# Kernel optimization log

Measured on AMD Instinct MI355X. Metric: run time of the kernel, lower is better.

Reference implementation:

```python
import jax, jax.numpy as jnp
import numpy as np
import math

D_MODEL = 1024
D_HEAD = 128
B, T = 4, 4096


def setup_inputs() -> dict:
    key = jax.random.key(0)
    ks = jax.random.split(key, 7)
    x = jax.random.normal(ks[0], (B, T, D_MODEL), dtype=jnp.float32)
    # realistic RoPE tables for positions 0..T-1, d_head//2 frequencies
    half = D_HEAD // 2
    inv_freq = 1.0 / (10000.0 ** (np.arange(0, half, dtype=np.float32) / half))
    pos = np.arange(T, dtype=np.float32)
    ang = pos[:, None] * inv_freq[None, :]  # [T, half]
    cos = jnp.asarray(np.cos(ang), dtype=jnp.float32)
    sin = jnp.asarray(np.sin(ang), dtype=jnp.float32)
    scale = 1.0 / math.sqrt(D_MODEL)
    Wq = jax.random.normal(ks[1], (D_MODEL, D_HEAD), dtype=jnp.float32) * scale
    Wk = jax.random.normal(ks[2], (D_MODEL, D_HEAD), dtype=jnp.float32) * scale
    Wv = jax.random.normal(ks[3], (D_MODEL, D_HEAD), dtype=jnp.float32) * scale
    gamma = jnp.zeros((D_HEAD,), dtype=jnp.float32)
    return {"x": x, "cos": cos, "sin": sin, "Wq": Wq, "Wk": Wk, "Wv": Wv, "gamma": gamma}


def _rotary(t, cos, sin):
    # t: [B, T, d_head]; cos/sin: [T, d_head//2]
    t1 = t[..., ::2]
    t2 = t[..., 1::2]
    r1 = t1 * cos - t2 * sin
    r2 = t1 * sin + t2 * cos
    # interleave back: stack on new last axis then flatten
    return jnp.stack([r1, r2], axis=-1).reshape(t.shape)


def reference(x, cos, sin, Wq, Wk, Wv, gamma):
    d_head = Wq.shape[-1]
    Q = x @ Wq  # [B, T, d_head]
    K = x @ Wk
    V = x @ Wv
    Qr = _rotary(Q, cos, sin)
    Kr = _rotary(K, cos, sin)
    gate = jnp.exp(gamma)  # SPD gate
    Qr = Qr * gate
    Kr = Kr * gate
    scores = jnp.einsum('btd,bsd->bts', Qr, Kr) / math.sqrt(d_head)
    attn = jax.nn.softmax(scores, axis=-1)
    out = jnp.einsum('bts,bsd->btd', attn, V)
    return out
```

## Files before the change

kernel.cpp:

```cpp
#include <hip/hip_runtime.h>

typedef _Float16 h8  __attribute__((ext_vector_type(8)));
typedef float f32x16 __attribute__((ext_vector_type(16)));

#define L2E 1.4426950408889634f

__device__ __forceinline__ void gll16(const void* g, void* l) {
  __builtin_amdgcn_global_load_lds((const __attribute__((address_space(1))) void*)g,
                                   (__attribute__((address_space(3))) void*)l, 16, 0, 0);
}

__global__ void k_cvt_x(const float* __restrict__ x, _Float16* __restrict__ xh) {
  int i = (blockIdx.x * 256 + threadIdx.x) * 8;
  float4 a = *(const float4*)(x + i);
  float4 b = *(const float4*)(x + i + 4);
  h8 o;
  o[0] = (_Float16)a.x; o[1] = (_Float16)a.y; o[2] = (_Float16)a.z; o[3] = (_Float16)a.w;
  o[4] = (_Float16)b.x; o[5] = (_Float16)b.y; o[6] = (_Float16)b.z; o[7] = (_Float16)b.w;
  *(h8*)(xh + i) = o;
}

__global__ void k_cvt_w(const float* __restrict__ Wq, const float* __restrict__ Wk,
                        const float* __restrict__ Wv, _Float16* __restrict__ WT) {
  int id = blockIdx.x * 256 + threadIdx.x;
  int mat = id >> 17;
  int rem = id & 131071;
  int k = rem >> 7;
  int c = rem & 127;
  const float* W = (mat == 0) ? Wq : ((mat == 1) ? Wk : Wv);
  WT[mat * 131072 + c * 1024 + k] = (_Float16)W[rem];
}

__global__ __launch_bounds__(256, 2) void k_proj(
    const _Float16* __restrict__ xh,
    const _Float16* __restrict__ WT,
    const float* __restrict__ cosT, const float* __restrict__ sinT,
    const float* __restrict__ gamma,
    _Float16* __restrict__ Qh, _Float16* __restrict__ Kh, _Float16* __restrict__ VT) {
  __shared__ __align__(16) unsigned char lds[65536];
  const int tid = threadIdx.x;
  const int rt  = blockIdx.x & 127;
  const int mat = blockIdx.x >> 7;
  const int w = tid >> 6, lane = tid & 63;
  const int wr = w >> 1, wc = w & 1;
  const int r32 = lane & 31, h = lane >> 5;
  const int row0 = rt * 128;
  const _Float16* Wbase = WT + mat * 131072;

  auto stage = [&](int j) {
    int k0 = j * 64;
    unsigned char* xb = lds + (j & 1) * 32768;
    unsigned char* wb = xb + 16384;
#pragma unroll
    for (int ii = 0; ii < 4; ++ii) {
      int off = ii * 4096 + tid * 16;
      int r = off >> 7;
      int c = (off >> 4) & 7;
      gll16(xh + (size_t)(row0 + r) * 1024 + k0 + ((c ^ (r & 7)) * 8), xb + off);
    }
#pragma unroll
    for (int ii = 0; ii < 4; ++ii) {
      int off = ii * 4096 + tid * 16;
      int r = off >> 7;
      int c = (off >> 4) & 7;
      gll16(Wbase + (size_t)r * 1024 + k0 + ((c ^ (r & 7)) * 8), wb + off);
    }
  };

  f32x16 acc[2][2];
#pragma unroll
  for (int a_ = 0; a_ < 2; ++a_)
#pragma unroll
    for (int b_ = 0; b_ < 2; ++b_)
#pragma unroll
      for (int r = 0; r < 16; ++r) acc[a_][b_][r] = 0.f;

  stage(0);
  for (int j = 0; j < 16; ++j) {
    if (j < 15) {
      stage(j + 1);
      asm volatile("s_waitcnt vmcnt(8)\n\ts_barrier" ::: "memory");
    } else {
      asm volatile("s_waitcnt vmcnt(0)\n\ts_barrier" ::: "memory");
    }
    const _Float16* xt = (const _Float16*)(lds + (j & 1) * 32768);
    const _Float16* wt = xt + 8192;
#pragma unroll
    for (int kk = 0; kk < 4; ++kk) {
      h8 a0, a1, b0, b1;
      { int r = wr * 64 + r32;      a0 = *(const h8*)(xt + r * 64 + (((kk * 2 + h) ^ (r & 7)) * 8)); }
      { int r = wr * 64 + 32 + r32; a1 = *(const h8*)(xt + r * 64 + (((kk * 2 + h) ^ (r & 7)) * 8)); }
      { int r = wc * 64 + r32;      b0 = *(const h8*)(wt + r * 64 + (((kk * 2 + h) ^ (r & 7)) * 8)); }
      { int r = wc * 64 + 32 + r32; b1 = *(const h8*)(wt + r * 64 + (((kk * 2 + h) ^ (r & 7)) * 8)); }
      acc[0][0] = __builtin_amdgcn_mfma_f32_32x32x16_f16(a0, b0, acc[0][0], 0, 0, 0);
      acc[0][1] = __builtin_amdgcn_mfma_f32_32x32x16_f16(a0, b1, acc[0][1], 0, 0, 0);
      acc[1][0] = __builtin_amdgcn_mfma_f32_32x32x16_f16(a1, b0, acc[1][0], 0, 0, 0);
      acc[1][1] = __builtin_amdgcn_mfma_f32_32x32x16_f16(a1, b1, acc[1][1], 0, 0, 0);
    }
    asm volatile("s_waitcnt lgkmcnt(0)\n\ts_barrier" ::: "memory");
  }

#pragma unroll
  for (int mt = 0; mt < 2; ++mt)
#pragma unroll
    for (int nt = 0; nt < 2; ++nt) {
      int col = wc * 64 + nt * 32 + r32;
      f32x16 c = acc[mt][nt];
      if (mat < 2) {
        float ge = expf(gamma[col]);
        float sc = (mat == 0) ? ge * 0.08838834764831845f : ge;
        int i2 = col >> 1;
#pragma unroll
        for (int rg = 0; rg < 16; ++rg) {
          int row = row0 + wr * 64 + mt * 32 + (rg & 3) + 8 * (rg >> 2) + 4 * h;
          int pos = row & 4095;
          float cv = cosT[pos * 64 + i2], sv = sinT[pos * 64 + i2];
          float val = c[rg];
          float ot = __shfl_xor(val, 1);
          float rr = (lane & 1) ? fmaf(val, cv, ot * sv) : fmaf(val, cv, -ot * sv);
          float v = rr * sc;
          if (mat == 0) {
            Qh[(size_t)row * 128 + col] = (_Float16)v;
          } else {
            size_t ka = (size_t)(row >> 5) * 4096 + (col >> 4) * 512 +
                        ((col >> 3) & 1) * 256 + (row & 31) * 8 + (col & 7);
            Kh[ka] = (_Float16)v;
          }
        }
      } else {
#pragma unroll
        for (int g = 0; g < 4; ++g) {
          union { _Float16 hh[4]; uint2 u; } pk;
#pragma unroll
          for (int j2 = 0; j2 < 4; ++j2) pk.hh[j2] = (_Float16)c[g * 4 + j2];
          int kv = row0 + wr * 64 + mt * 32 + 8 * g + 4 * h;
          size_t va = (size_t)(kv >> 5) * 4096 +
                      ((col >> 5) * 2 + ((kv >> 4) & 1)) * 512 +
                      ((kv >> 3) & 1) * 256 + (col & 31) * 8 + (kv & 7);
          *(uint2*)(VT + va) = pk.u;
        }
      }
    }
}

__global__ __launch_bounds__(512, 2) void k_attn(
    const _Float16* __restrict__ Qh, const _Float16* __restrict__ Kh,
    const _Float16* __restrict__ VT, float* __restrict__ out) {
  extern __shared__ __align__(16) unsigned char lds_raw[];
  const int tid = threadIdx.x;
  const int bid = blockIdx.x;
  const int xcd = bid & 7;
  const int b  = xcd >> 1;
  const int q0 = ((xcd & 1) + 2 * (bid >> 3)) * 64;
  const int w = tid >> 6, lane = tid & 63;
  const int wk = w >> 1, wq = w & 1;
  const int r32 = lane & 31, h = lane >> 5;

  const _Float16* qrow = Qh + (size_t)(b * 4096 + q0 + wq * 32 + r32) * 128;
  h8 qf[8];
#pragma unroll
  for (int kk = 0; kk < 8; ++kk) qf[kk] = *(const h8*)(qrow + kk * 16 + h * 8);

  const _Float16* Kfb = Kh + (size_t)(b * 128 + wk) * 4096 + lane * 8;
  const _Float16* Vfb = VT + (size_t)(b * 128 + wk) * 4096 + lane * 8;

  f32x16 o_acc[4];
#pragma unroll
  for (int dt = 0; dt < 4; ++dt)
#pragma unroll
    for (int r = 0; r < 16; ++r) o_acc[dt][r] = 0.f;
  float mcur = -INFINITY, lsum = 0.f;

  h8 kf[8];
#pragma unroll
  for (int kk = 0; kk < 8; ++kk) kf[kk] = *(const h8*)(Kfb + kk * 512);

  for (int i = 0; i < 32; ++i) {
    __builtin_amdgcn_s_barrier();

    const _Float16* Vcur = Vfb + (size_t)i * 16384;
    h8 vf[8];
#pragma unroll
    for (int u = 0; u < 8; ++u) vf[u] = *(const h8*)(Vcur + u * 512);

    const _Float16* Knext = Kfb + (size_t)(i + 1) * 16384;
    f32x16 st0, st1;
#pragma unroll
    for (int r = 0; r < 16; ++r) { st0[r] = 0.f; st1[r] = 0.f; }
    __builtin_amdgcn_s_setprio(1);
#pragma unroll
    for (int kk = 0; kk < 8; ++kk) {
      h8 a = kf[kk];
      if (i < 31) kf[kk] = *(const h8*)(Knext + kk * 512);
      if (kk & 1) st1 = __builtin_amdgcn_mfma_f32_32x32x16_f16(a, qf[kk], st1, 0, 0, 0);
      else        st0 = __builtin_amdgcn_mfma_f32_32x32x16_f16(a, qf[kk], st0, 0, 0, 0);
    }
    __builtin_amdgcn_s_setprio(0);
    f32x16 st = st0 + st1;

    float pm = fmaxf(fmaxf(fmaxf(st[0], st[1]), fmaxf(st[2], st[3])),
                     fmaxf(fmaxf(st[4], st[5]), fmaxf(st[6], st[7])));
    float pm2 = fmaxf(fmaxf(fmaxf(st[8], st[9]), fmaxf(st[10], st[11])),
                      fmaxf(fmaxf(st[12], st[13]), fmaxf(st[14], st[15])));
    pm = fmaxf(pm, pm2);
    pm = fmaxf(pm, __shfl_xor(pm, 32));
    if (!__all(pm - mcur <= 8.0f)) {
      float mnew = fmaxf(mcur, pm);
      float fsc = exp2f((mcur - mnew) * L2E);
      lsum *= fsc;
#pragma unroll
      for (int dt = 0; dt < 4; ++dt) o_acc[dt] = o_acc[dt] * fsc;
      mcur = mnew;
    }
    float mn2 = mcur * L2E;
    float pv[16]; float ps = 0.f;
#pragma unroll
    for (int r = 0; r < 16; ++r) { pv[r] = exp2f(fmaf(st[r], L2E, -mn2)); ps += pv[r]; }
    ps += __shfl_xor(ps, 32);
    lsum += ps;

    unsigned int wrd[8], owd[8];
#pragma unroll
    for (int t8 = 0; t8 < 8; ++t8) {
      auto hp = __builtin_amdgcn_cvt_pkrtz(pv[2 * t8], pv[2 * t8 + 1]);
      wrd[t8] = __builtin_bit_cast(unsigned int, hp);
    }
#pragma unroll
    for (int t8 = 0; t8 < 8; ++t8) owd[t8] = (unsigned int)__shfl_xor((int)wrd[t8], 32);
    const bool hb = (h != 0);
    __builtin_amdgcn_s_setprio(1);
#pragma unroll
    for (int kvb = 0; kvb < 2; ++kvb) {
      union { unsigned int u[4]; h8 v; } pb;
      pb.u[0] = hb ? owd[4 * kvb + 2] : wrd[4 * kvb + 0];
      pb.u[1] = hb ? owd[4 * kvb + 3] : wrd[4 * kvb + 1];
      pb.u[2] = hb ? wrd[4 * kvb + 2] : owd[4 * kvb + 0];
      pb.u[3] = hb ? wrd[4 * kvb + 3] : owd[4 * kvb + 1];
#pragma unroll
      for (int dt = 0; dt < 4; ++dt)
        o_acc[dt] = __builtin_amdgcn_mfma_f32_32x32x16_f16(vf[dt * 2 + kvb], pb.v, o_acc[dt], 0, 0, 0);
    }
    __builtin_amdgcn_s_setprio(0);
  }

  __syncthreads();
  float* MB = (float*)lds_raw;
  float* ML = (float*)(lds_raw + 98304);
  if (wk >= 1) {
    int si = wk - 1;
#pragma unroll
    for (int dt = 0; dt < 4; ++dt)
#pragma unroll
      for (int rg = 0; rg < 16; ++rg)
        MB[(((si * 2 + wq) * 64) + dt * 16 + rg) * 64 + lane] = o_acc[dt][rg];
    if (lane < 32) {
      ML[(si * 2 + wq) * 64 + lane] = mcur;
      ML[(si * 2 + wq) * 64 + 32 + lane] = lsum;
    }
  }
  __syncthreads();
  if (wk == 0) {
#pragma unroll
    for (int si = 0; si < 3; ++si) {
      float m1 = ML[(si * 2 + wq) * 64 + r32];
      float l1 = ML[(si * 2 + wq) * 64 + 32 + r32];
      float ms = fmaxf(mcur, m1);
      float f0 = exp2f((mcur - ms) * L2E), f1 = exp2f((m1 - ms) * L2E);
#pragma unroll
      for (int dt = 0; dt < 4; ++dt)
#pragma unroll
        for (int rg = 0; rg < 16; ++rg)
          o_acc[dt][rg] = o_acc[dt][rg] * f0 +
                          MB[(((si * 2 + wq) * 64) + dt * 16 + rg) * 64 + lane] * f1;
      lsum = lsum * f0 + l1 * f1;
      mcur = ms;
    }
    float inv = 1.0f / lsum;
#pragma unroll
    for (int dt = 0; dt < 4; ++dt) o_acc[dt] = o_acc[dt] * inv;
  }
  __syncthreads();
  float* OT = (float*)lds_raw;
  if (wk == 0) {
#pragma unroll
    for (int dt = 0; dt < 4; ++dt)
#pragma unroll
      for (int rg = 0; rg < 16; ++rg) {
        int d = dt * 32 + (rg & 3) + 8 * (rg >> 2) + 4 * h;
        OT[(wq * 32 + r32) * 129 + d] = o_acc[dt][rg];
      }
  }
  __syncthreads();
#pragma unroll
  for (int pi = 0; pi < 16; ++pi) {
    int idx = pi * 512 + tid;
    int qr = idx >> 7, c = idx & 127;
    out[(size_t)(b * 4096 + q0 + qr) * 128 + c] = OT[qr * 129 + c];
  }
}

extern "C" void kernel_launch(void* const* d_in, const int* in_sizes, int n_in,
                              void* d_out, int out_size, void* d_ws, size_t ws_size,
                              hipStream_t stream) {
  const float* x     = (const float*)d_in[0];
  const float* cosT  = (const float*)d_in[1];
  const float* sinT  = (const float*)d_in[2];
  const float* Wq    = (const float*)d_in[3];
  const float* Wk    = (const float*)d_in[4];
  const float* Wv    = (const float*)d_in[5];
  const float* gamma = (const float*)d_in[6];
  char* ws = (char*)d_ws;
  _Float16* xh = (_Float16*)(ws);
  _Float16* WT = (_Float16*)(ws + 33554432);
  _Float16* Qh = (_Float16*)(ws + 34340864);
  _Float16* Kh = (_Float16*)(ws + 38535168);
  _Float16* VT = (_Float16*)(ws + 42729472);
  float* out = (float*)d_out;

  (void)hipFuncSetAttribute(reinterpret_cast<const void*>(k_attn),
                            hipFuncAttributeMaxDynamicSharedMemorySize, 131072);

  hipLaunchKernelGGL(k_cvt_x, dim3(8192), dim3(256), 0, stream, x, xh);
  hipLaunchKernelGGL(k_cvt_w, dim3(1536), dim3(256), 0, stream, Wq, Wk, Wv, WT);
  hipLaunchKernelGGL(k_proj, dim3(384), dim3(256), 0, stream, xh, WT, cosT, sinT, gamma, Qh, Kh, VT);
  hipLaunchKernelGGL(k_attn, dim3(256), dim3(512), 131072, stream, Qh, Kh, VT, out);
}
```

Baseline: 113.6 us.

## Split attention KV range across eight wave pairs with tree reduction

Doubles the attention block to 1024 threads so eight KV-split groups each process 16 tiles instead of four groups processing 32, and drops the per-iteration barrier. The final merge now computes the global max and sum once, rescales each partial, then sums partial outputs through LDS in a three-level tree. This shortens each wave's serial KV loop and the merge chain, at the cost of more register pressure per thread under the 1024-thread launch bound and more LDS reduction passes.

```diff
diff --git a/kernel.cpp b/kernel.cpp
--- a/kernel.cpp
+++ b/kernel.cpp
@@ -143,7 +143,7 @@
     }
 }
 
-__global__ __launch_bounds__(512, 2) void k_attn(
+__global__ __launch_bounds__(1024) void k_attn(
     const _Float16* __restrict__ Qh, const _Float16* __restrict__ Kh,
     const _Float16* __restrict__ VT, float* __restrict__ out) {
   extern __shared__ __align__(16) unsigned char lds_raw[];
@@ -152,8 +152,8 @@
   const int xcd = bid & 7;
   const int b  = xcd >> 1;
   const int q0 = ((xcd & 1) + 2 * (bid >> 3)) * 64;
-  const int w = tid >> 6, lane = tid & 63;
-  const int wk = w >> 1, wq = w & 1;
+  const int wid = tid >> 6, lane = tid & 63;
+  const int s = wid >> 1, wq = wid & 1;
   const int r32 = lane & 31, h = lane >> 5;
 
   const _Float16* qrow = Qh + (size_t)(b * 4096 + q0 + wq * 32 + r32) * 128;
@@ -161,8 +161,9 @@
 #pragma unroll
   for (int kk = 0; kk < 8; ++kk) qf[kk] = *(const h8*)(qrow + kk * 16 + h * 8);
 
-  const _Float16* Kfb = Kh + (size_t)(b * 128 + wk) * 4096 + lane * 8;
-  const _Float16* Vfb = VT + (size_t)(b * 128 + wk) * 4096 + lane * 8;
+  const size_t TSTRIDE = 8 * 4096;
+  const _Float16* Kfb = Kh + (size_t)(b * 128 + s) * 4096 + lane * 8;
+  const _Float16* Vfb = VT + (size_t)(b * 128 + s) * 4096 + lane * 8;
 
   f32x16 o_acc[4];
 #pragma unroll
@@ -175,15 +176,13 @@
 #pragma unroll
   for (int kk = 0; kk < 8; ++kk) kf[kk] = *(const h8*)(Kfb + kk * 512);
 
-  for (int i = 0; i < 32; ++i) {
-    __builtin_amdgcn_s_barrier();
-
-    const _Float16* Vcur = Vfb + (size_t)i * 16384;
+  for (int i = 0; i < 16; ++i) {
+    const _Float16* Vcur = Vfb + (size_t)i * TSTRIDE;
     h8 vf[8];
 #pragma unroll
     for (int u = 0; u < 8; ++u) vf[u] = *(const h8*)(Vcur + u * 512);
 
-    const _Float16* Knext = Kfb + (size_t)(i + 1) * 16384;
+    const _Float16* Kn = Kfb + (size_t)(i + 1) * TSTRIDE;
     f32x16 st0, st1;
 #pragma unroll
     for (int r = 0; r < 16; ++r) { st0[r] = 0.f; st1[r] = 0.f; }
@@ -191,7 +190,7 @@
 #pragma unroll
     for (int kk = 0; kk < 8; ++kk) {
       h8 a = kf[kk];
-      if (i < 31) kf[kk] = *(const h8*)(Knext + kk * 512);
+      if (i < 15) kf[kk] = *(const h8*)(Kn + kk * 512);
       if (kk & 1) st1 = __builtin_amdgcn_mfma_f32_32x32x16_f16(a, qf[kk], st1, 0, 0, 0);
       else        st0 = __builtin_amdgcn_mfma_f32_32x32x16_f16(a, qf[kk], st0, 0, 0, 0);
     }
@@ -243,45 +242,62 @@
     __builtin_amdgcn_s_setprio(0);
   }
 
-  __syncthreads();
+  float* ML = (float*)lds_raw;
+  if (lane < 32) {
+    ML[wid * 64 + lane] = mcur;
+    ML[wid * 64 + 32 + lane] = lsum;
+  }
+  __syncthreads();
+  float mstar = -INFINITY;
+  float msv[8], lsv[8];
+#pragma unroll
+  for (int s2 = 0; s2 < 8; ++s2) {
+    msv[s2] = ML[(s2 * 2 + wq) * 64 + r32];
+    lsv[s2] = ML[(s2 * 2 + wq) * 64 + 32 + r32];
+    mstar = fmaxf(mstar, msv[s2]);
+  }
+  float L = 0.f;
+#pragma unroll
+  for (int s2 = 0; s2 < 8; ++s2) L += lsv[s2] * exp2f((msv[s2] - mstar) * L2E);
+  float fown = exp2f((msv[s] - mstar) * L2E);
+  float inv = 1.0f / L;
+#pragma unroll
+  for (int dt = 0; dt < 4; ++dt) o_acc[dt] = o_acc[dt] * fown;
+  __syncthreads();
+
   float* MB = (float*)lds_raw;
-  float* ML = (float*)(lds_raw + 98304);
-  if (wk >= 1) {
-    int si = wk - 1;
+  auto mbw = [&](int slot) {
+    float* p = MB + (size_t)((slot * 2 + wq) * 64) * 64;
 #pragma unroll
     for (int dt = 0; dt < 4; ++dt)
 #pragma unroll
-      for (int rg = 0; rg < 16; ++rg)
-        MB[(((si * 2 + wq) * 64) + dt * 16 + rg) * 64 + lane] = o_acc[dt][rg];
-    if (lane < 32) {
-      ML[(si * 2 + wq) * 64 + lane] = mcur;
-      ML[(si * 2 + wq) * 64 + 32 + lane] = lsum;
-    }
-  }
-  __syncthreads();
-  if (wk == 0) {
-#pragma unroll
-    for (int si = 0; si < 3; ++si) {
-      float m1 = ML[(si * 2 + wq) * 64 + r32];
-      float l1 = ML[(si * 2 + wq) * 64 + 32 + r32];
-      float ms = fmaxf(mcur, m1);
-      float f0 = exp2f((mcur - ms) * L2E), f1 = exp2f((m1 - ms) * L2E);
-#pragma unroll
-      for (int dt = 0; dt < 4; ++dt)
-#pragma unroll
-        for (int rg = 0; rg < 16; ++rg)
-          o_acc[dt][rg] = o_acc[dt][rg] * f0 +
-                          MB[(((si * 2 + wq) * 64) + dt * 16 + rg) * 64 + lane] * f1;
-      lsum = lsum * f0 + l1 * f1;
-      mcur = ms;
-    }
-    float inv = 1.0f / lsum;
+      for (int rg = 0; rg < 16; ++rg) p[(dt * 16 + rg) * 64 + lane] = o_acc[dt][rg];
+  };
+  auto mba = [&](int slot) {
+    float* p = MB + (size_t)((slot * 2 + wq) * 64) * 64;
+#pragma unroll
+    for (int dt = 0; dt < 4; ++dt)
+#pragma unroll
+      for (int rg = 0; rg < 16; ++rg) o_acc[dt][rg] += p[(dt * 16 + rg) * 64 + lane];
+  };
+  if (s >= 4) mbw(s - 4);
+  __syncthreads();
+  if (s < 4) mba(s);
+  __syncthreads();
+  if (s == 2 || s == 3) mbw(s - 2);
+  __syncthreads();
+  if (s < 2) mba(s);
+  __syncthreads();
+  if (s == 1) mbw(0);
+  __syncthreads();
+  if (s == 0) {
+    mba(0);
 #pragma unroll
     for (int dt = 0; dt < 4; ++dt) o_acc[dt] = o_acc[dt] * inv;
   }
   __syncthreads();
   float* OT = (float*)lds_raw;
-  if (wk == 0) {
+  if (s == 0) {
 #pragma unroll
     for (int dt = 0; dt < 4; ++dt)
 #pragma unroll
@@ -292,8 +308,8 @@
   }
   __syncthreads();
 #pragma unroll
-  for (int pi = 0; pi < 16; ++pi) {
-    int idx = pi * 512 + tid;
+  for (int pi = 0; pi < 8; ++pi) {
+    int idx = pi * 1024 + tid;
     int qr = idx >> 7, c = idx & 127;
     out[(size_t)(b * 4096 + q0 + qr) * 128 + c] = OT[qr * 129 + c];
   }
@@ -323,5 +339,5 @@
   hipLaunchKernelGGL(k_cvt_x, dim3(8192), dim3(256), 0, stream, x, xh);
   hipLaunchKernelGGL(k_cvt_w, dim3(1536), dim3(256), 0, stream, Wq, Wk, Wv, WT);
   hipLaunchKernelGGL(k_proj, dim3(384), dim3(256), 0, stream, xh, WT, cosT, sinT, gamma, Qh, Kh, VT);
-  hipLaunchKernelGGL(k_attn, dim3(256), dim3(512), 131072, stream, Qh, Kh, VT, out);
-}
+  hipLaunchKernelGGL(k_attn, dim3(256), dim3(1024), 131072, stream, Qh, Kh, VT, out);
+}
```

Result: slower. 411.6 us (+262.2%).
